# Performance work log

Measured on AMD Instinct MI355X. Metric: run time of the kernel, lower is better.

## Reference

```python
import jax, jax.numpy as jnp
import numpy as np

N_NODES = 50000
N_EDGES = 1_600_000
FEAT, HIDDEN, NUM_CLASS = 128, 128, 64


def setup_inputs() -> dict:
    key = jax.random.key(0)
    k1, k2, k3, k4, k5 = jax.random.split(key, 5)
    h = jax.random.normal(k1, (N_NODES, FEAT), dtype=jnp.float32)
    edge_index = jax.random.randint(k2, (2, N_EDGES), 0, N_NODES, dtype=jnp.int32)
    # Glorot-ish init for the three GraphConv weights (bias=False)
    W1 = jax.random.normal(k3, (FEAT, HIDDEN), dtype=jnp.float32) * (1.0 / np.sqrt(FEAT))
    W2 = jax.random.normal(k4, (HIDDEN, HIDDEN), dtype=jnp.float32) * (1.0 / np.sqrt(HIDDEN))
    W3 = jax.random.normal(k5, (HIDDEN, NUM_CLASS), dtype=jnp.float32) * (1.0 / np.sqrt(HIDDEN))
    return {"h": h, "edge_index": edge_index, "W1": W1, "W2": W2, "W3": W3}


def _gcn_layer(h, W, src, dst, out_isqrt, in_isqrt, n_nodes):
    # DGL GraphConv, norm='both', bias=False: relu( D_in^{-1/2} A D_out^{-1/2} h W )
    h = h * out_isqrt[:, None]          # scale source features
    h = h @ W                            # dense projection (order-invariant)
    agg = jax.ops.segment_sum(h[src], dst, num_segments=n_nodes)  # SpMM aggregation
    agg = agg * in_isqrt[:, None]
    return jax.nn.relu(agg)


def reference(h, edge_index, W1, W2, W3):
    src, dst = edge_index[0], edge_index[1]
    ones = jnp.ones(src.shape[0], dtype=h.dtype)
    out_deg = jax.ops.segment_sum(ones, src, num_segments=N_NODES)
    in_deg = jax.ops.segment_sum(ones, dst, num_segments=N_NODES)
    out_isqrt = jnp.clip(out_deg, 1.0, None) ** -0.5
    in_isqrt = jnp.clip(in_deg, 1.0, None) ** -0.5
    h = _gcn_layer(h, W1, src, dst, out_isqrt, in_isqrt, N_NODES)
    h = _gcn_layer(h, W2, src, dst, out_isqrt, in_isqrt, N_NODES)
    h = _gcn_layer(h, W3, src, dst, out_isqrt, in_isqrt, N_NODES)
    return h
```

## Files before the change

kernel.cpp:

```cpp
#include <hip/hip_runtime.h>

#define N_NODES 50000
#define N_EDGES 1600000
#define FEAT 128
#define HIDDEN 128
#define NUM_CLASS 64

#define NBUCK 782
#define EPB 2048
#define NBLK 782
#define SCAP 2560
#define AGG_NBN 3125
#define GEMM_BLOCKS 782
#define NSHW 6256

typedef _Float16 h8 __attribute__((ext_vector_type(8)));
typedef _Float16 h4 __attribute__((ext_vector_type(4)));
typedef float f32x4 __attribute__((ext_vector_type(4)));

__global__ __launch_bounds__(256) void passA_kernel(const int* __restrict__ ei,
                                                    unsigned* __restrict__ priv,
                                                    int* __restrict__ localoff,
                                                    int* __restrict__ Cmat,
                                                    unsigned* __restrict__ nibshad,
                                                    const float* __restrict__ W1,
                                                    const float* __restrict__ W2,
                                                    const float* __restrict__ W3,
                                                    _Float16* __restrict__ WhT) {
    const int t = threadIdx.x;
    const int blk = blockIdx.x;
    if (blk >= NBLK) {
        const int id = (blk - NBLK) * 256 + t;
        if (id < 16384) {
            const int n = id >> 7, k = id & 127;
            WhT[id] = (_Float16)W1[k * 128 + n];
        } else if (id < 32768) {
            const int i = id - 16384, n = i >> 7, k = i & 127;
            WhT[id] = (_Float16)W2[k * 128 + n];
        } else if (id < 40960) {
            const int i = id - 32768, n = i >> 7, k = i & 127;
            WhT[id] = (_Float16)W3[k * 64 + n];
        }
        return;
    }
    __shared__ int cnt[1024];
    __shared__ int base[1024];
    __shared__ int cur[1024];
    __shared__ int tmp[256];
    __shared__ unsigned sorted[EPB];
    __shared__ unsigned nib[NSHW];
    for (int i = t; i < 1024; i += 256) cnt[i] = 0;
    for (int i = t; i < NSHW; i += 256) nib[i] = 0;
    __syncthreads();

    const int ebase = blk * EPB;
    unsigned packed[8];
    int bk[8];
#pragma unroll
    for (int j = 0; j < 8; ++j) {
        const int e = ebase + t + j * 256;
        if (e < N_EDGES) {
            const unsigned s = (unsigned)ei[e];
            const unsigned d = (unsigned)ei[N_EDGES + e];
            bk[j] = (int)(d >> 6);
            packed[j] = s | ((d & 63u) << 16) | ((d >> 6) << 22);
            atomicAdd(&cnt[bk[j]], 1);
            atomicAdd(&nib[s >> 3], 1u << ((s & 7u) * 4u));
        } else bk[j] = -1;
    }
    __syncthreads();

    const int c0 = cnt[4*t], c1 = cnt[4*t+1], c2 = cnt[4*t+2], c3 = cnt[4*t+3];
    const int s = c0 + c1 + c2 + c3;
    tmp[t] = s;
    __syncthreads();
    for (int off = 1; off < 256; off <<= 1) {
        int v = (t >= off) ? tmp[t - off] : 0;
        __syncthreads();
        tmp[t] += v;
        __syncthreads();
    }
    const int excl = tmp[t] - s;
    base[4*t] = excl;            cur[4*t] = excl;
    base[4*t+1] = excl+c0;       cur[4*t+1] = excl+c0;
    base[4*t+2] = excl+c0+c1;    cur[4*t+2] = excl+c0+c1;
    base[4*t+3] = excl+c0+c1+c2; cur[4*t+3] = excl+c0+c1+c2;
    __syncthreads();

    for (int b = t; b < NBUCK; b += 256) {
        localoff[(size_t)blk * NBUCK + b] = base[b];
        Cmat[(size_t)blk * NBUCK + b] = cnt[b];
    }
#pragma unroll
    for (int j = 0; j < 8; ++j)
        if (bk[j] >= 0) {
            const int pos = atomicAdd(&cur[bk[j]], 1);
            sorted[pos] = packed[j];
        }
    __syncthreads();
    const int total = min(EPB, N_EDGES - ebase);
    for (int i = t; i < total; i += 256) priv[(size_t)blk * EPB + i] = sorted[i];
    unsigned* dst = nibshad + (size_t)blk * NSHW;
    for (int i = t; i < NSHW; i += 256) dst[i] = nib[i];
}

__global__ __launch_bounds__(256) void setup_kernel(const int* __restrict__ Cmat,
                                                    int* __restrict__ total,
                                                    const unsigned* __restrict__ nibshad,
                                                    float* __restrict__ out_isqrt) {
    const int bid = blockIdx.x;
    const int t = threadIdx.x;
    if (bid < 196) {
        const int b0 = bid * 4;
        const int c = t & 3, r = t >> 2;
        int s = 0;
        if (b0 + c < NBUCK)
            for (int i = r; i < NBLK; i += 64) s += Cmat[(size_t)i * NBUCK + b0 + c];
        __shared__ int red[256];
        red[t] = s;
        __syncthreads();
        for (int off = 128; off >= 4; off >>= 1) {
            if (t < off) red[t] += red[t + off];
            __syncthreads();
        }
        if (t < 4 && b0 + t < NBUCK) total[b0 + t] = red[t];
        return;
    }
    const int blk = bid - 196;
    const int w0 = blk * 8;
    const int wl = t & 7, c = t >> 3;
    int acc[8] = {0, 0, 0, 0, 0, 0, 0, 0};
    for (int sh = c; sh < NBLK; sh += 32) {
        const unsigned u = nibshad[(size_t)sh * NSHW + w0 + wl];
        acc[0] += u & 15u;         acc[1] += (u >> 4) & 15u;
        acc[2] += (u >> 8) & 15u;  acc[3] += (u >> 12) & 15u;
        acc[4] += (u >> 16) & 15u; acc[5] += (u >> 20) & 15u;
        acc[6] += (u >> 24) & 15u; acc[7] += (u >> 28);
    }
    __shared__ int red2[32][8][8];
#pragma unroll
    for (int nb = 0; nb < 8; ++nb) red2[c][wl][nb] = acc[nb];
    __syncthreads();
    for (int off = 16; off > 0; off >>= 1) {
        if (c < off) {
#pragma unroll
            for (int nb = 0; nb < 8; ++nb) red2[c][wl][nb] += red2[c + off][wl][nb];
        }
        __syncthreads();
    }
    if (t < 64) {
        const int wl2 = t >> 3, nb = t & 7;
        const int node = (w0 + wl2) * 8 + nb;
        if (node < N_NODES) {
            const int d = red2[0][wl2][nb];
            out_isqrt[node] = rsqrtf((float)(d < 1 ? 1 : d));
        }
    }
}

template <int OUT, typename InT>
__device__ __forceinline__ void gemm_body(const InT* __restrict__ H,
                                          const _Float16* __restrict__ WhT,
                                          const float* __restrict__ out_isqrt,
                                          _Float16* __restrict__ Ys,
                                          const int bidx, const int tid,
                                          _Float16* Hs) {
    constexpr int NT = OUT / 16;
    char* hb = (char*)Hs;
    const int bn = bidx * 64;

    {
        const int n = tid & 63, kg = tid >> 6;
        const int gn = bn + n;
        const int swz = (n & 7) << 4;
        if (gn < N_NODES) {
            if constexpr (sizeof(InT) == 4) {
                const float4* hrow = (const float4*)(H + (size_t)gn * FEAT) + kg * 8;
#pragma unroll
                for (int jj = 0; jj < 4; ++jj) {
                    const float4 u = hrow[jj * 2];
                    const float4 v = hrow[jj * 2 + 1];
                    h8 r;
                    r[0] = (_Float16)u.x; r[1] = (_Float16)u.y; r[2] = (_Float16)u.z; r[3] = (_Float16)u.w;
                    r[4] = (_Float16)v.x; r[5] = (_Float16)v.y; r[6] = (_Float16)v.z; r[7] = (_Float16)v.w;
                    *(h8*)(hb + ((n * 256 + kg * 64 + jj * 16) ^ swz)) = r;
                }
            } else {
                const h8* hrow = (const h8*)(H + (size_t)gn * FEAT) + kg * 4;
#pragma unroll
                for (int jj = 0; jj < 4; ++jj)
                    *(h8*)(hb + ((n * 256 + kg * 64 + jj * 16) ^ swz)) = hrow[jj];
            }
        } else {
            h8 z;
#pragma unroll
            for (int i = 0; i < 8; ++i) z[i] = (_Float16)0.f;
#pragma unroll
            for (int jj = 0; jj < 4; ++jj)
                *(h8*)(hb + ((n * 256 + kg * 64 + jj * 16) ^ swz)) = z;
        }
    }
    __syncthreads();

    const int l = tid & 63, w = tid >> 6;
    const int lm = l & 15, lk = l >> 4;
    const int nloc = w * 16 + lm;
    const int swzr = (nloc & 7) << 4;

    h8 bfrag[4];
#pragma unroll
    for (int kt = 0; kt < 4; ++kt)
        bfrag[kt] = *(const h8*)(hb + ((nloc * 256 + (lk * 8 + kt * 32) * 2) ^ swzr));

    f32x4 acc[NT];
#pragma unroll
    for (int nt = 0; nt < NT; ++nt) acc[nt] = (f32x4){0.f, 0.f, 0.f, 0.f};

#pragma unroll
    for (int nt = 0; nt < NT; ++nt) {
        const _Float16* wp = WhT + (size_t)(nt * 16 + lm) * 128 + lk * 8;
#pragma unroll
        for (int kt = 0; kt < 4; ++kt) {
            const h8 afrag = *(const h8*)(wp + kt * 32);
            acc[nt] = __builtin_amdgcn_mfma_f32_16x16x32_f16(afrag, bfrag[kt], acc[nt], 0, 0, 0);
        }
    }

    const int node = bn + w * 16 + lm;
    if (node < N_NODES) {
        const float sc = out_isqrt[node];
#pragma unroll
        for (int nt = 0; nt < NT; ++nt) {
            const int f0 = nt * 16 + lk * 4;
            h4 r;
            r[0] = (_Float16)(acc[nt][0] * sc);
            r[1] = (_Float16)(acc[nt][1] * sc);
            r[2] = (_Float16)(acc[nt][2] * sc);
            r[3] = (_Float16)(acc[nt][3] * sc);
            *(h4*)(Ys + ((size_t)(f0 >> 5) * N_NODES + node) * 32 + (f0 & 31)) = r;
        }
    }
}

template <int OUT, typename InT>
__global__ __launch_bounds__(256) void gemm_kernel(const InT* __restrict__ H,
                                                   const _Float16* __restrict__ WhT,
                                                   const float* __restrict__ out_isqrt,
                                                   _Float16* __restrict__ Ys) {
    __shared__ _Float16 Hs[64 * 128];
    gemm_body<OUT, InT>(H, WhT, out_isqrt, Ys, blockIdx.x, threadIdx.x, Hs);
}

__global__ __launch_bounds__(256) void csr2gemm_kernel(const int* __restrict__ localoff,
                                                       const unsigned* __restrict__ priv,
                                                       const int* __restrict__ total,
                                                       unsigned short* __restrict__ csr,
                                                       int* __restrict__ row_off,
                                                       float* __restrict__ in_isqrt,
                                                       const float* __restrict__ H,
                                                       const _Float16* __restrict__ WhT,
                                                       const float* __restrict__ out_isqrt,
                                                       _Float16* __restrict__ Ys) {
    __shared__ char smem[16384];
    const int bid = blockIdx.x;
    const int t = threadIdx.x;
    if (bid >= NBUCK) {
        gemm_body<HIDDEN, float>(H, WhT, out_isqrt, Ys, bid - NBUCK, t, (_Float16*)smem);
        return;
    }
    int* tmp = (int*)smem;
    unsigned* gath = (unsigned*)(smem + 1024);
    int* cnt64 = (int*)(smem + 1024 + SCAP * 4);
    int* cur64 = cnt64 + 64;
    const int b = bid;

    {
        const int g = 4 * t;
        const int s0 = (g < NBUCK) ? total[g] : 0;
        const int s1 = (g + 1 < NBUCK) ? total[g + 1] : 0;
        const int s2 = (g + 2 < NBUCK) ? total[g + 2] : 0;
        const int s3 = (g + 3 < NBUCK) ? total[g + 3] : 0;
        const int s = s0 + s1 + s2 + s3;
        tmp[t] = s;
        __syncthreads();
        for (int off = 1; off < 256; off <<= 1) {
            int v = (t >= off) ? tmp[t - off] : 0;
            __syncthreads();
            tmp[t] += v;
            __syncthreads();
        }
        const int excl = tmp[t] - s;
        __syncthreads();
        tmp[t] = excl;
        __syncthreads();
    }
    int cb = tmp[b >> 2];
    for (int u = (b & ~3); u < b; ++u) cb += total[u];
    __syncthreads();

    int off_[4], len_[4];
#pragma unroll
    for (int u = 0; u < 4; ++u) {
        const int blk = 4 * t + u;
        if (blk < NBLK) {
            const int o = localoff[(size_t)blk * NBUCK + b];
            const int nxt = (b == NBUCK - 1) ? min(EPB, N_EDGES - blk * EPB)
                                             : localoff[(size_t)blk * NBUCK + b + 1];
            off_[u] = o; len_[u] = nxt - o;
        } else { off_[u] = 0; len_[u] = 0; }
    }
    const int s = len_[0] + len_[1] + len_[2] + len_[3];
    tmp[t] = s;
    __syncthreads();
    for (int off = 1; off < 256; off <<= 1) {
        int v = (t >= off) ? tmp[t - off] : 0;
        __syncthreads();
        tmp[t] += v;
        __syncthreads();
    }
    int run = tmp[t] - s;
    const int totalE = tmp[255];
#pragma unroll
    for (int u = 0; u < 4; ++u) {
        const int blk = 4 * t + u;
        const unsigned* srcp = priv + (size_t)blk * EPB + off_[u];
        for (int j = 0; j < len_[u]; ++j)
            if (run + j < SCAP) gath[run + j] = srcp[j];
        run += len_[u];
    }
    if (t < 64) cnt64[t] = 0;
    __syncthreads();

    const int gtot = min(totalE, SCAP);
    for (int i = t; i < gtot; i += 256) atomicAdd(&cnt64[(gath[i] >> 16) & 63u], 1);
    __syncthreads();

    const int v64 = (t < 64) ? cnt64[t] : 0;
    tmp[t] = v64;
    __syncthreads();
    for (int off = 1; off < 64; off <<= 1) {
        int v = (t >= off) ? tmp[t - off] : 0;
        __syncthreads();
        tmp[t] += v;
        __syncthreads();
    }
    if (t < 64) {
        const int myoff = cb + tmp[t] - v64;
        cur64[t] = myoff;
        const int node = b * 64 + t;
        if (node < N_NODES) {
            row_off[node] = myoff;
            in_isqrt[node] = rsqrtf((float)(v64 > 0 ? v64 : 1));
        }
    }
    if (bid == 0 && t == 0) row_off[N_NODES] = N_EDGES;
    __syncthreads();

    for (int i = t; i < gtot; i += 256) {
        const unsigned w = gath[i];
        const int pos = atomicAdd(&cur64[(w >> 16) & 63u], 1);
        csr[pos] = (unsigned short)(w & 0xFFFFu);
    }
}

template <int F, typename OT>
__global__ __launch_bounds__(256) void agg_kernel(const int* __restrict__ row_off,
                                                  const unsigned short* __restrict__ csr,
                                                  const _Float16* __restrict__ Ys,
                                                  const float* __restrict__ in_isqrt,
                                                  OT* __restrict__ out) {
    constexpr int NS = F / 32;
    const int s  = blockIdx.x & (NS - 1);
    const int nb = blockIdx.x / NS;
    const int tid = threadIdx.x;
    const int lane = tid & 63;
    const int j = lane >> 4;
    const int esub = (lane >> 2) & 3;
    const int q = lane & 3;

    const int d = nb * 16 + (tid >> 6) * 4 + j;
    const _Float16* Yp = Ys + (size_t)s * (N_NODES * 32) + q * 8;

    const int end = row_off[d + 1];
    float a0 = 0.f, a1 = 0.f, a2 = 0.f, a3 = 0.f, a4 = 0.f, a5 = 0.f, a6 = 0.f, a7 = 0.f;

    int e = row_off[d] + esub;
    for (; e + 12 < end; e += 16) {
        const int i0 = csr[e];
        const int i1 = csr[e + 4];
        const int i2 = csr[e + 8];
        const int i3 = csr[e + 12];
        const h8 v0 = *(const h8*)(Yp + (size_t)i0 * 32);
        const h8 v1 = *(const h8*)(Yp + (size_t)i1 * 32);
        const h8 v2 = *(const h8*)(Yp + (size_t)i2 * 32);
        const h8 v3 = *(const h8*)(Yp + (size_t)i3 * 32);
        a0 += (float)v0[0] + (float)v1[0] + (float)v2[0] + (float)v3[0];
        a1 += (float)v0[1] + (float)v1[1] + (float)v2[1] + (float)v3[1];
        a2 += (float)v0[2] + (float)v1[2] + (float)v2[2] + (float)v3[2];
        a3 += (float)v0[3] + (float)v1[3] + (float)v2[3] + (float)v3[3];
        a4 += (float)v0[4] + (float)v1[4] + (float)v2[4] + (float)v3[4];
        a5 += (float)v0[5] + (float)v1[5] + (float)v2[5] + (float)v3[5];
        a6 += (float)v0[6] + (float)v1[6] + (float)v2[6] + (float)v3[6];
        a7 += (float)v0[7] + (float)v1[7] + (float)v2[7] + (float)v3[7];
    }
    for (; e + 4 < end; e += 8) {
        const int i0 = csr[e];
        const int i1 = csr[e + 4];
        const h8 v0 = *(const h8*)(Yp + (size_t)i0 * 32);
        const h8 v1 = *(const h8*)(Yp + (size_t)i1 * 32);
        a0 += (float)v0[0] + (float)v1[0];
        a1 += (float)v0[1] + (float)v1[1];
        a2 += (float)v0[2] + (float)v1[2];
        a3 += (float)v0[3] + (float)v1[3];
        a4 += (float)v0[4] + (float)v1[4];
        a5 += (float)v0[5] + (float)v1[5];
        a6 += (float)v0[6] + (float)v1[6];
        a7 += (float)v0[7] + (float)v1[7];
    }
    if (e < end) {
        const int i0 = csr[e];
        const h8 v0 = *(const h8*)(Yp + (size_t)i0 * 32);
        a0 += (float)v0[0]; a1 += (float)v0[1]; a2 += (float)v0[2]; a3 += (float)v0[3];
        a4 += (float)v0[4]; a5 += (float)v0[5]; a6 += (float)v0[6]; a7 += (float)v0[7];
    }

    a0 += __shfl_xor(a0, 4, 64); a0 += __shfl_xor(a0, 8, 64);
    a1 += __shfl_xor(a1, 4, 64); a1 += __shfl_xor(a1, 8, 64);
    a2 += __shfl_xor(a2, 4, 64); a2 += __shfl_xor(a2, 8, 64);
    a3 += __shfl_xor(a3, 4, 64); a3 += __shfl_xor(a3, 8, 64);
    a4 += __shfl_xor(a4, 4, 64); a4 += __shfl_xor(a4, 8, 64);
    a5 += __shfl_xor(a5, 4, 64); a5 += __shfl_xor(a5, 8, 64);
    a6 += __shfl_xor(a6, 4, 64); a6 += __shfl_xor(a6, 8, 64);
    a7 += __shfl_xor(a7, 4, 64); a7 += __shfl_xor(a7, 8, 64);

    if (esub == 0) {
        const float isq = in_isqrt[d];
        const float r0 = fmaxf(a0 * isq, 0.f), r1 = fmaxf(a1 * isq, 0.f);
        const float r2 = fmaxf(a2 * isq, 0.f), r3 = fmaxf(a3 * isq, 0.f);
        const float r4 = fmaxf(a4 * isq, 0.f), r5 = fmaxf(a5 * isq, 0.f);
        const float r6 = fmaxf(a6 * isq, 0.f), r7 = fmaxf(a7 * isq, 0.f);
        if constexpr (sizeof(OT) == 2) {
            h8 o;
            o[0] = (_Float16)r0; o[1] = (_Float16)r1; o[2] = (_Float16)r2; o[3] = (_Float16)r3;
            o[4] = (_Float16)r4; o[5] = (_Float16)r5; o[6] = (_Float16)r6; o[7] = (_Float16)r7;
            *(h8*)((_Float16*)out + (size_t)d * F + s * 32 + q * 8) = o;
        } else {
            float* op = (float*)out + (size_t)d * F + s * 32 + q * 8;
            float4 w0 = {r0, r1, r2, r3}, w1 = {r4, r5, r6, r7};
            *(float4*)op = w0;
            *(float4*)(op + 4) = w1;
        }
    }
}

extern "C" void kernel_launch(void* const* d_in, const int* in_sizes, int n_in,
                              void* d_out, int out_size, void* d_ws, size_t ws_size,
                              hipStream_t stream) {
    const float* h  = (const float*)d_in[0];
    const int*   ei = (const int*)d_in[1];
    const float* W1 = (const float*)d_in[2];
    const float* W2 = (const float*)d_in[3];
    const float* W3 = (const float*)d_in[4];
    float* out = (float*)d_out;

    char* p = (char*)d_ws;
    auto alloc = [&p](size_t bytes) {
        void* r = (void*)p;
        p += (bytes + 255) & ~(size_t)255;
        return r;
    };
    int*   row_off  = (int*)alloc((N_NODES + 1) * sizeof(int));
    int*   total    = (int*)alloc(NBUCK * sizeof(int));
    unsigned short* csr = (unsigned short*)alloc((size_t)N_EDGES * sizeof(unsigned short));
    float* in_isqrt  = (float*)alloc(N_NODES * sizeof(float));
    float* out_isqrt = (float*)alloc(N_NODES * sizeof(float));
    _Float16* WhT   = (_Float16*)alloc(40960 * sizeof(_Float16));
    _Float16* Ys    = (_Float16*)alloc((size_t)N_NODES * HIDDEN * sizeof(_Float16));
    _Float16* bufA  = (_Float16*)alloc((size_t)N_NODES * HIDDEN * sizeof(_Float16));
    _Float16* bufB  = (_Float16*)alloc((size_t)N_NODES * HIDDEN * sizeof(_Float16));
    unsigned* nibshad = (unsigned*)alloc((size_t)NBLK * NSHW * sizeof(unsigned));
    unsigned* priv   = (unsigned*)bufA;
    int* localoff    = (int*)bufB;
    int* Cmat        = localoff + (size_t)NBLK * NBUCK;

    passA_kernel<<<NBLK + 160, 256, 0, stream>>>(ei, priv, localoff, Cmat, nibshad,
                                                 W1, W2, W3, WhT);
    setup_kernel<<<978, 256, 0, stream>>>(Cmat, total, nibshad, out_isqrt);
    csr2gemm_kernel<<<NBUCK + GEMM_BLOCKS, 256, 0, stream>>>(localoff, priv, total,
                                                             csr, row_off, in_isqrt,
                                                             h, WhT, out_isqrt, Ys);

    agg_kernel<HIDDEN, _Float16><<<4 * AGG_NBN, 256, 0, stream>>>(row_off, csr, Ys, in_isqrt, bufA);

    gemm_kernel<HIDDEN, _Float16><<<GEMM_BLOCKS, 256, 0, stream>>>(bufA, WhT + 16384, out_isqrt, Ys);
    agg_kernel<HIDDEN, _Float16><<<4 * AGG_NBN, 256, 0, stream>>>(row_off, csr, Ys, in_isqrt, bufB);

    gemm_kernel<NUM_CLASS, _Float16><<<GEMM_BLOCKS, 256, 0, stream>>>(bufB, WhT + 32768, out_isqrt, Ys);
    agg_kernel<NUM_CLASS, float><<<2 * AGG_NBN, 256, 0, stream>>>(row_off, csr, Ys, in_isqrt, out);
}
```

Before: 216.2 us.

## Fuse aggregation with next-layer GEMM and switch Y to row-major layout

Merges each layer's SpMM aggregation with the following layer's MFMA projection into one kernel. Each 1024-thread block aggregates 16 destination nodes into shared memory, then multiplies them by the next weight matrix. The intermediate Y is now stored row-major instead of split into 32-feature slabs, so each gather reads a full contiguous row. This drops two GEMM launches and the round trip of intermediate activations through global memory. In exchange, blocks are larger and an extra barrier is added, the 4-way unrolled gather loop is removed, and one wave handles all edges of a node, which may reduce latency hiding.

```diff
diff --git a/kernel.cpp b/kernel.cpp
--- a/kernel.cpp
+++ b/kernel.cpp
@@ -10,7 +10,6 @@
 #define EPB 2048
 #define NBLK 782
 #define SCAP 2560
-#define AGG_NBN 3125
 #define GEMM_BLOCKS 782
 #define NSHW 6256
 
@@ -162,7 +161,7 @@
 __device__ __forceinline__ void gemm_body(const InT* __restrict__ H,
                                           const _Float16* __restrict__ WhT,
                                           const float* __restrict__ out_isqrt,
-                                          _Float16* __restrict__ Ys,
+                                          _Float16* __restrict__ Yout,
                                           const int bidx, const int tid,
                                           _Float16* Hs) {
     constexpr int NT = OUT / 16;
@@ -237,18 +236,9 @@
             r[1] = (_Float16)(acc[nt][1] * sc);
             r[2] = (_Float16)(acc[nt][2] * sc);
             r[3] = (_Float16)(acc[nt][3] * sc);
-            *(h4*)(Ys + ((size_t)(f0 >> 5) * N_NODES + node) * 32 + (f0 & 31)) = r;
-        }
-    }
-}
-
-template <int OUT, typename InT>
-__global__ __launch_bounds__(256) void gemm_kernel(const InT* __restrict__ H,
-                                                   const _Float16* __restrict__ WhT,
-                                                   const float* __restrict__ out_isqrt,
-                                                   _Float16* __restrict__ Ys) {
-    __shared__ _Float16 Hs[64 * 128];
-    gemm_body<OUT, InT>(H, WhT, out_isqrt, Ys, blockIdx.x, threadIdx.x, Hs);
+            *(h4*)(Yout + (size_t)node * OUT + f0) = r;
+        }
+    }
 }
 
 __global__ __launch_bounds__(256) void csr2gemm_kernel(const int* __restrict__ localoff,
@@ -363,51 +353,33 @@
     }
 }
 
-template <int F, typename OT>
-__global__ __launch_bounds__(256) void agg_kernel(const int* __restrict__ row_off,
-                                                  const unsigned short* __restrict__ csr,
-                                                  const _Float16* __restrict__ Ys,
-                                                  const float* __restrict__ in_isqrt,
-                                                  OT* __restrict__ out) {
-    constexpr int NS = F / 32;
-    const int s  = blockIdx.x & (NS - 1);
-    const int nb = blockIdx.x / NS;
+template <int OUT>
+__global__ __launch_bounds__(1024) void agg_gemm_kernel(const int* __restrict__ row_off,
+                                                        const unsigned short* __restrict__ csr,
+                                                        const _Float16* __restrict__ Ys,
+                                                        const float* __restrict__ in_isqrt,
+                                                        const float* __restrict__ out_isqrt,
+                                                        const _Float16* __restrict__ WhT,
+                                                        _Float16* __restrict__ Yout) {
+    __shared__ _Float16 A[16 * 128];
+    char* ab = (char*)A;
     const int tid = threadIdx.x;
+    const int w = tid >> 6;
     const int lane = tid & 63;
-    const int j = lane >> 4;
-    const int esub = (lane >> 2) & 3;
-    const int q = lane & 3;
-
-    const int d = nb * 16 + (tid >> 6) * 4 + j;
-    const _Float16* Yp = Ys + (size_t)s * (N_NODES * 32) + q * 8;
-
+    const int q = lane & 15;
+    const int esub = lane >> 4;
+    const int d = blockIdx.x * 16 + w;
+
+    const _Float16* Yp = Ys + q * 8;
     const int end = row_off[d + 1];
     float a0 = 0.f, a1 = 0.f, a2 = 0.f, a3 = 0.f, a4 = 0.f, a5 = 0.f, a6 = 0.f, a7 = 0.f;
 
     int e = row_off[d] + esub;
-    for (; e + 12 < end; e += 16) {
-        const int i0 = csr[e];
-        const int i1 = csr[e + 4];
-        const int i2 = csr[e + 8];
-        const int i3 = csr[e + 12];
-        const h8 v0 = *(const h8*)(Yp + (size_t)i0 * 32);
-        const h8 v1 = *(const h8*)(Yp + (size_t)i1 * 32);
-        const h8 v2 = *(const h8*)(Yp + (size_t)i2 * 32);
-        const h8 v3 = *(const h8*)(Yp + (size_t)i3 * 32);
-        a0 += (float)v0[0] + (float)v1[0] + (float)v2[0] + (float)v3[0];
-        a1 += (float)v0[1] + (float)v1[1] + (float)v2[1] + (float)v3[1];
-        a2 += (float)v0[2] + (float)v1[2] + (float)v2[2] + (float)v3[2];
-        a3 += (float)v0[3] + (float)v1[3] + (float)v2[3] + (float)v3[3];
-        a4 += (float)v0[4] + (float)v1[4] + (float)v2[4] + (float)v3[4];
-        a5 += (float)v0[5] + (float)v1[5] + (float)v2[5] + (float)v3[5];
-        a6 += (float)v0[6] + (float)v1[6] + (float)v2[6] + (float)v3[6];
-        a7 += (float)v0[7] + (float)v1[7] + (float)v2[7] + (float)v3[7];
-    }
     for (; e + 4 < end; e += 8) {
         const int i0 = csr[e];
         const int i1 = csr[e + 4];
-        const h8 v0 = *(const h8*)(Yp + (size_t)i0 * 32);
-        const h8 v1 = *(const h8*)(Yp + (size_t)i1 * 32);
+        const h8 v0 = *(const h8*)(Yp + (size_t)i0 * 128);
+        const h8 v1 = *(const h8*)(Yp + (size_t)i1 * 128);
         a0 += (float)v0[0] + (float)v1[0];
         a1 += (float)v0[1] + (float)v1[1];
         a2 += (float)v0[2] + (float)v1[2];
@@ -419,37 +391,97 @@
     }
     if (e < end) {
         const int i0 = csr[e];
-        const h8 v0 = *(const h8*)(Yp + (size_t)i0 * 32);
+        const h8 v0 = *(const h8*)(Yp + (size_t)i0 * 128);
         a0 += (float)v0[0]; a1 += (float)v0[1]; a2 += (float)v0[2]; a3 += (float)v0[3];
         a4 += (float)v0[4]; a5 += (float)v0[5]; a6 += (float)v0[6]; a7 += (float)v0[7];
     }
 
-    a0 += __shfl_xor(a0, 4, 64); a0 += __shfl_xor(a0, 8, 64);
-    a1 += __shfl_xor(a1, 4, 64); a1 += __shfl_xor(a1, 8, 64);
-    a2 += __shfl_xor(a2, 4, 64); a2 += __shfl_xor(a2, 8, 64);
-    a3 += __shfl_xor(a3, 4, 64); a3 += __shfl_xor(a3, 8, 64);
-    a4 += __shfl_xor(a4, 4, 64); a4 += __shfl_xor(a4, 8, 64);
-    a5 += __shfl_xor(a5, 4, 64); a5 += __shfl_xor(a5, 8, 64);
-    a6 += __shfl_xor(a6, 4, 64); a6 += __shfl_xor(a6, 8, 64);
-    a7 += __shfl_xor(a7, 4, 64); a7 += __shfl_xor(a7, 8, 64);
+    a0 += __shfl_xor(a0, 16, 64); a0 += __shfl_xor(a0, 32, 64);
+    a1 += __shfl_xor(a1, 16, 64); a1 += __shfl_xor(a1, 32, 64);
+    a2 += __shfl_xor(a2, 16, 64); a2 += __shfl_xor(a2, 32, 64);
+    a3 += __shfl_xor(a3, 16, 64); a3 += __shfl_xor(a3, 32, 64);
+    a4 += __shfl_xor(a4, 16, 64); a4 += __shfl_xor(a4, 32, 64);
+    a5 += __shfl_xor(a5, 16, 64); a5 += __shfl_xor(a5, 32, 64);
+    a6 += __shfl_xor(a6, 16, 64); a6 += __shfl_xor(a6, 32, 64);
+    a7 += __shfl_xor(a7, 16, 64); a7 += __shfl_xor(a7, 32, 64);
 
     if (esub == 0) {
         const float isq = in_isqrt[d];
-        const float r0 = fmaxf(a0 * isq, 0.f), r1 = fmaxf(a1 * isq, 0.f);
-        const float r2 = fmaxf(a2 * isq, 0.f), r3 = fmaxf(a3 * isq, 0.f);
-        const float r4 = fmaxf(a4 * isq, 0.f), r5 = fmaxf(a5 * isq, 0.f);
-        const float r6 = fmaxf(a6 * isq, 0.f), r7 = fmaxf(a7 * isq, 0.f);
-        if constexpr (sizeof(OT) == 2) {
-            h8 o;
-            o[0] = (_Float16)r0; o[1] = (_Float16)r1; o[2] = (_Float16)r2; o[3] = (_Float16)r3;
-            o[4] = (_Float16)r4; o[5] = (_Float16)r5; o[6] = (_Float16)r6; o[7] = (_Float16)r7;
-            *(h8*)((_Float16*)out + (size_t)d * F + s * 32 + q * 8) = o;
-        } else {
-            float* op = (float*)out + (size_t)d * F + s * 32 + q * 8;
-            float4 w0 = {r0, r1, r2, r3}, w1 = {r4, r5, r6, r7};
-            *(float4*)op = w0;
-            *(float4*)(op + 4) = w1;
-        }
+        h8 r;
+        r[0] = (_Float16)fmaxf(a0 * isq, 0.f); r[1] = (_Float16)fmaxf(a1 * isq, 0.f);
+        r[2] = (_Float16)fmaxf(a2 * isq, 0.f); r[3] = (_Float16)fmaxf(a3 * isq, 0.f);
+        r[4] = (_Float16)fmaxf(a4 * isq, 0.f); r[5] = (_Float16)fmaxf(a5 * isq, 0.f);
+        r[6] = (_Float16)fmaxf(a6 * isq, 0.f); r[7] = (_Float16)fmaxf(a7 * isq, 0.f);
+        *(h8*)(ab + ((w * 256 + q * 16) ^ ((w & 7) << 4))) = r;
+    }
+    __syncthreads();
+
+    if (w < OUT / 16) {
+        const int lm = lane & 15, lk = lane >> 4;
+        const int swzr = (lm & 7) << 4;
+        h8 bfrag[4];
+#pragma unroll
+        for (int kt = 0; kt < 4; ++kt)
+            bfrag[kt] = *(const h8*)(ab + ((lm * 256 + (lk * 8 + kt * 32) * 2) ^ swzr));
+
+        f32x4 acc = (f32x4){0.f, 0.f, 0.f, 0.f};
+        const _Float16* wp = WhT + (size_t)(w * 16 + lm) * 128 + lk * 8;
+#pragma unroll
+        for (int kt = 0; kt < 4; ++kt) {
+            const h8 afrag = *(const h8*)(wp + kt * 32);
+            acc = __builtin_amdgcn_mfma_f32_16x16x32_f16(afrag, bfrag[kt], acc, 0, 0, 0);
+        }
+        const int node = blockIdx.x * 16 + lm;
+        const float sc = out_isqrt[node];
+        const int f0 = w * 16 + lk * 4;
+        h4 r;
+        r[0] = (_Float16)(acc[0] * sc); r[1] = (_Float16)(acc[1] * sc);
+        r[2] = (_Float16)(acc[2] * sc); r[3] = (_Float16)(acc[3] * sc);
+        *(h4*)(Yout + (size_t)node * OUT + f0) = r;
+    }
+}
+
+__global__ __launch_bounds__(256) void agg_final_kernel(const int* __restrict__ row_off,
+                                                        const unsigned short* __restrict__ csr,
+                                                        const _Float16* __restrict__ Ys,
+                                                        const float* __restrict__ in_isqrt,
+                                                        float* __restrict__ out) {
+    const int tid = threadIdx.x;
+    const int lane = tid & 63;
+    const int q = lane & 7;
+    const int esub = lane >> 3;
+    const int d = blockIdx.x * 4 + (tid >> 6);
+
+    const _Float16* Yp = Ys + q * 8;
+    const int end = row_off[d + 1];
+    float a0 = 0.f, a1 = 0.f, a2 = 0.f, a3 = 0.f, a4 = 0.f, a5 = 0.f, a6 = 0.f, a7 = 0.f;
+
+    for (int e = row_off[d] + esub; e < end; e += 8) {
+        const int i0 = csr[e];
+        const h8 v0 = *(const h8*)(Yp + (size_t)i0 * 64);
+        a0 += (float)v0[0]; a1 += (float)v0[1]; a2 += (float)v0[2]; a3 += (float)v0[3];
+        a4 += (float)v0[4]; a5 += (float)v0[5]; a6 += (float)v0[6]; a7 += (float)v0[7];
+    }
+
+    a0 += __shfl_xor(a0, 8, 64); a0 += __shfl_xor(a0, 16, 64); a0 += __shfl_xor(a0, 32, 64);
+    a1 += __shfl_xor(a1, 8, 64); a1 += __shfl_xor(a1, 16, 64); a1 += __shfl_xor(a1, 32, 64);
+    a2 += __shfl_xor(a2, 8, 64); a2 += __shfl_xor(a2, 16, 64); a2 += __shfl_xor(a2, 32, 64);
+    a3 += __shfl_xor(a3, 8, 64); a3 += __shfl_xor(a3, 16, 64); a3 += __shfl_xor(a3, 32, 64);
+    a4 += __shfl_xor(a4, 8, 64); a4 += __shfl_xor(a4, 16, 64); a4 += __shfl_xor(a4, 32, 64);
+    a5 += __shfl_xor(a5, 8, 64); a5 += __shfl_xor(a5, 16, 64); a5 += __shfl_xor(a5, 32, 64);
+    a6 += __shfl_xor(a6, 8, 64); a6 += __shfl_xor(a6, 16, 64); a6 += __shfl_xor(a6, 32, 64);
+    a7 += __shfl_xor(a7, 8, 64); a7 += __shfl_xor(a7, 16, 64); a7 += __shfl_xor(a7, 32, 64);
+
+    if (esub == 0) {
+        const float isq = in_isqrt[d];
+        float4 r0, r1;
+        r0.x = fmaxf(a0 * isq, 0.f); r0.y = fmaxf(a1 * isq, 0.f);
+        r0.z = fmaxf(a2 * isq, 0.f); r0.w = fmaxf(a3 * isq, 0.f);
+        r1.x = fmaxf(a4 * isq, 0.f); r1.y = fmaxf(a5 * isq, 0.f);
+        r1.z = fmaxf(a6 * isq, 0.f); r1.w = fmaxf(a7 * isq, 0.f);
+        float* op = out + (size_t)d * NUM_CLASS + q * 8;
+        *(float4*)op = r0;
+        *(float4*)(op + 4) = r1;
     }
 }
 
@@ -490,11 +522,9 @@
                                                              csr, row_off, in_isqrt,
                                                              h, WhT, out_isqrt, Ys);
 
-    agg_kernel<HIDDEN, _Float16><<<4 * AGG_NBN, 256, 0, stream>>>(row_off, csr, Ys, in_isqrt, bufA);
-
-    gemm_kernel<HIDDEN, _Float16><<<GEMM_BLOCKS, 256, 0, stream>>>(bufA, WhT + 16384, out_isqrt, Ys);
-    agg_kernel<HIDDEN, _Float16><<<4 * AGG_NBN, 256, 0, stream>>>(row_off, csr, Ys, in_isqrt, bufB);
-
-    gemm_kernel<NUM_CLASS, _Float16><<<GEMM_BLOCKS, 256, 0, stream>>>(bufB, WhT + 32768, out_isqrt, Ys);
-    agg_kernel<NUM_CLASS, float><<<2 * AGG_NBN, 256, 0, stream>>>(row_off, csr, Ys, in_isqrt, out);
-}
+    agg_gemm_kernel<HIDDEN><<<3125, 1024, 0, stream>>>(row_off, csr, Ys, in_isqrt,
+                                                       out_isqrt, WhT + 16384, bufA);
+    agg_gemm_kernel<NUM_CLASS><<<3125, 1024, 0, stream>>>(row_off, csr, bufA, in_isqrt,
+                                                          out_isqrt, WhT + 32768, bufB);
+    agg_final_kernel<<<12500, 256, 0, stream>>>(row_off, csr, bufB, in_isqrt, out);
+}
```

After: 229.5 us. 6.2% more time.
